# Kernel tuning notes

Hardware: AMD Instinct MI355X
Metric: run time of the kernel (lower is better)

The kernel has to match this reference:

```python
import jax, jax.numpy as jnp
import numpy as np
import math
from jax import lax

NUM_POS = 128        # random_choice in pos_neg_sampling
NUM_TOT = 256        # pos + (128 + negative_padding) always totals 256
POS_W = 10.0         # positive_weight in compute_loss


def _conv(x, w, b, pad):
    y = lax.conv_general_dilated(x, w, (1, 1), pad,
                                 dimension_numbers=('NCHW', 'OIHW', 'NCHW'))
    return y + b[None, :, None, None]


def make_anchor_box(img_h, img_w, gh, gw):
    # torch.range(0, W, W/(gw-1)) == inclusive linspace with gw points
    xs = jnp.linspace(0.0, float(img_w), gw)
    ys = jnp.linspace(0.0, float(img_h), gh)
    gx, gy = jnp.meshgrid(xs, ys, indexing='ij')          # (gw, gh) like torch.meshgrid
    xy = jnp.stack([gx.reshape(-1), gy.reshape(-1)], -1).reshape(gh, gw, 2)
    whs = []
    for area in (128 * 128, 256 * 256, 512 * 512):
        for wr, hr in ((1, 1), (2, 1), (1, 2)):
            u = math.sqrt(area / (wr * hr))
            whs.append((wr * u, hr * u))
    wh = jnp.asarray(whs, jnp.float32)                    # (9, 2)
    xy9 = jnp.broadcast_to(xy[:, :, None, :], (gh, gw, 9, 2))
    wh9 = jnp.broadcast_to(wh[None, None], (gh, gw, 9, 2))
    boxes = jnp.concatenate([xy9, xy9 + wh9], -1)         # x1,y1,x2,y2
    return boxes.reshape(-1, 4)


def pairwise_iou(t, a):
    # t: [T,4], a: [A,4], xyxy -> [T,A]
    lt = jnp.maximum(t[:, None, :2], a[None, :, :2])
    rb = jnp.minimum(t[:, None, 2:], a[None, :, 2:])
    wh = jnp.clip(rb - lt, 0.0)
    inter = wh[..., 0] * wh[..., 1]
    at = (t[:, 2] - t[:, 0]) * (t[:, 3] - t[:, 1])
    aa = (a[:, 2] - a[:, 0]) * (a[:, 3] - a[:, 1])
    return inter / (at[:, None] + aa[None, :] - inter)


def box_encode(anchor, bbox):
    awh = anchor[:, 2:] - anchor[:, :2]
    bwh = bbox[:, 2:] - bbox[:, :2]
    ac = anchor[:, :2] + awh / 2
    bc = bbox[:, :2] + bwh / 2
    dxy = (bc - ac) / awh
    dwh = jnp.log(bwh / awh)
    return jnp.concatenate([dxy, dwh], 1)


def rpn_forward(x, target, conv_w, conv_b, bbox_w, bbox_b, score_w, score_b,
                img_h, img_w):
    gh, gw = x.shape[-2], x.shape[-1]
    h = jax.nn.relu(_conv(x[None], conv_w, conv_b, 'SAME'))
    bbox = jax.nn.relu(_conv(h, bbox_w, bbox_b, 'VALID')).reshape(-1, 4)   # [A,4]
    score = jax.nn.relu(_conv(h, score_w, score_b, 'VALID')).reshape(-1, 2)  # [A,2]
    anchors = make_anchor_box(img_h, img_w, gh, gw)                        # [A,4]

    iou = pairwise_iou(target, anchors)                                    # [T,A]
    max_iou = iou.max(0)
    tgt_idx = jnp.argmax(iou, 0)

    # deterministic replacement for np.random.choice sampling (fixed shapes)
    pos_score = jnp.where(max_iou > 0.7, max_iou, -1.0)
    pos_vals, pos_idx = lax.top_k(pos_score, NUM_POS)
    pos_valid = pos_vals > 0.0
    n_pos = jnp.sum(pos_valid.astype(jnp.int32))

    neg_score = jnp.where(max_iou < 0.3, 1.0 - max_iou, -1.0)
    neg_vals, neg_idx = lax.top_k(neg_score, NUM_TOT)
    neg_valid = (neg_vals > 0.0) & (jnp.arange(NUM_TOT) < (NUM_TOT - n_pos))

    bbox_pred = bbox[pos_idx]                                              # [128,4]
    scores_sel = score[jnp.concatenate([pos_idx, neg_idx])]                # [384,2]
    valid = jnp.concatenate([pos_valid, neg_valid]).astype(jnp.float32)

    tgt_scores = jnp.concatenate([
        jnp.tile(jnp.asarray([[1.0, 0.0]], jnp.float32), (NUM_POS, 1)),
        jnp.tile(jnp.asarray([[0.0, 1.0]], jnp.float32), (NUM_TOT, 1))], 0)

    matched = target[tgt_idx[pos_idx]]
    treg = box_encode(anchors[pos_idx], matched)

    ce = -jnp.sum(tgt_scores * jax.nn.log_softmax(scores_sel, -1), -1)
    score_loss = jnp.sum(ce * valid) / jnp.maximum(jnp.sum(valid), 1.0)

    d = bbox_pred - treg
    sl1 = jnp.where(jnp.abs(d) < 1.0, 0.5 * d * d, jnp.abs(d) - 0.5)
    pm = pos_valid.astype(jnp.float32)[:, None]
    reg_loss = jnp.sum(sl1 * pm) / jnp.maximum(jnp.sum(pm) * 4.0, 1.0)

    return score_loss + POS_W * reg_loss


def setup_inputs():
    key = jax.random.key(0)
    ks = jax.random.split(key, 8)
    cin, gh, gw, nt = 512, 128, 128, 64
    x = jax.random.normal(ks[0], (cin, gh, gw), jnp.float32)
    cxy = jax.random.uniform(ks[1], (nt, 2), minval=300.0, maxval=1748.0)
    wh = jax.random.uniform(ks[2], (nt, 2), minval=64.0, maxval=512.0)
    target = jnp.concatenate([cxy - wh / 2, cxy + wh / 2], -1)
    conv_w = jax.random.normal(ks[3], (cin, cin, 3, 3), jnp.float32) * 0.02
    conv_b = jnp.zeros((cin,), jnp.float32)
    bbox_w = jax.random.normal(ks[4], (36, cin, 1, 1), jnp.float32) * 0.02
    bbox_b = jnp.zeros((36,), jnp.float32)
    score_w = jax.random.normal(ks[5], (18, cin, 1, 1), jnp.float32) * 0.02
    score_b = jnp.zeros((18,), jnp.float32)
    return {'x': x, 'target': target, 'conv_w': conv_w, 'conv_b': conv_b,
            'bbox_w': bbox_w, 'bbox_b': bbox_b, 'score_w': score_w,
            'score_b': score_b, 'img_h': 2048, 'img_w': 2048}


def reference(x, target, conv_w, conv_b, bbox_w, bbox_b, score_w, score_b,
              img_h, img_w):
    return rpn_forward(x, target, conv_w, conv_b, bbox_w, bbox_b,
                       score_w, score_b, img_h, img_w)
```

## Files before the change

kernel.cpp:

```cpp
#include <hip/hip_runtime.h>
#include <cstdint>
#include <cstddef>

typedef unsigned long long ull;
typedef __bf16 bf16x8 __attribute__((ext_vector_type(8)));
typedef float f32x4 __attribute__((ext_vector_type(4)));

#define NA     147456
#define NT     64
#define KDIM   4608
#define NTASK  1280
#define CAND_CAP 4096
#define KSPLIT 2
#define NSTEP  72
#define NIOUB  576
#define NTRB   2048
#define NPREP2 512
#define NZERO  197

#define OFF_WB2   0
#define OFF_XT    4718592
#define OFF_ZERO  22024192
#define OFF_H4    22302720
#define OFF_MIOU  32788480
#define OFF_CAND  33378304
#define OFF_CPB   34557952
#define OFF_CBZ   34560256
#define OFF_NPOS  34562560
#define OFF_TREG  34562576
#define OFF_TASKS 34564624

#define UANC 90.509667991878f
__device__ __constant__ float WKa[9] = {128.0f, 2.0f*UANC, UANC, 256.0f, 4.0f*UANC, 2.0f*UANC, 512.0f, 8.0f*UANC, 4.0f*UANC};
__device__ __constant__ float HKa[9] = {128.0f, UANC, 2.0f*UANC, 256.0f, 2.0f*UANC, 4.0f*UANC, 512.0f, 4.0f*UANC, 8.0f*UANC};

__device__ __forceinline__ float iou_one(float x1, float y1, float x2, float y2, float4 t) {
#pragma clang fp contract(off)
  float ltx = fmaxf(t.x, x1), lty = fmaxf(t.y, y1);
  float rbx = fminf(t.z, x2), rby = fminf(t.w, y2);
  float wx = fmaxf(rbx - ltx, 0.0f);
  float wy = fmaxf(rby - lty, 0.0f);
  float inter = wx * wy;
  float at = (t.z - t.x) * (t.w - t.y);
  float aa = (x2 - x1) * (y2 - y1);
  return inter / ((at + aa) - inter);
}

__device__ __forceinline__ unsigned short f2bf(float f) {
  unsigned int u = __float_as_uint(f);
  unsigned int r = (u + 0x7fffu + ((u >> 16) & 1u)) >> 16;
  return (unsigned short)r;
}

__device__ __forceinline__ int boff(int kcb) {
  int rk = kcb >> 6;
  int dy = (rk * 11) >> 5;
  int dxo = rk - dy * 3;
  return (dy * 130 + dxo) * 512 + (kcb & 63) * 8;
}

__global__ __launch_bounds__(256) void k_pi(const float* __restrict__ cw,
    unsigned short* __restrict__ Wb2, const float* __restrict__ x,
    unsigned short* __restrict__ xtb, unsigned short* __restrict__ zrg,
    const float* __restrict__ tgt, const int* __restrict__ imw,
    const int* __restrict__ imh, float* __restrict__ miou,
    ull* __restrict__ cand, int* __restrict__ cpb, int* __restrict__ cbz,
    float* __restrict__ out0) {
  __shared__ __align__(16) char smem[20480];
  int blk = blockIdx.x;
  int tid = threadIdx.x;
  if (blk >= NIOUB + NTRB + NPREP2) {
    int g = (blk - (NIOUB + NTRB + NPREP2)) * 256 + tid;
    uint4 z = {0u, 0u, 0u, 0u};
    if (g == 0) *out0 = 0.0f;
    if (g < 17408) {
      *(uint4*)(zrg + g * 8) = z;
    } else {
      int h = g - 17408;
      int pixi = h >> 6, j = h & 63;
      int yy, xx;
      if (pixi < 260) { yy = (pixi < 130) ? 0 : 129; xx = (pixi < 130) ? pixi : pixi - 130; }
      else { int p2 = pixi - 260; if (p2 < 128) { yy = 1 + p2; xx = 0; } else { yy = p2 - 127; xx = 129; } }
      *(uint4*)(xtb + (size_t)(yy * 130 + xx) * 512 + j * 8) = z;
    }
    return;
  }
  if (blk >= NIOUB + NTRB) {
    float* row = (float*)smem;
    int m = blk - (NIOUB + NTRB);
    const float* src = cw + (size_t)m * KDIM;
    for (int f = tid; f < KDIM; f += 256) {
      int cin = f / 9;
      row[cin * 10 + (f - cin * 9)] = src[f];
    }
    __syncthreads();
    for (int kc = tid; kc < 576; kc += 256) {
      int r = kc >> 6, c8 = kc & 63;
      int base = c8 * 80 + r;
      unsigned short o[8];
      #pragma unroll
      for (int j = 0; j < 8; ++j) o[j] = f2bf(row[base + j * 10]);
      *(uint4*)(Wb2 + ((size_t)kc * 512 + m) * 8) = *(const uint4*)o;
    }
    return;
  }
  if (blk >= NIOUB) {
    float* tile = (float*)smem;
    int tb = blk - NIOUB;
    int pix0 = (tb & 255) * 64;
    int cin0 = (tb >> 8) * 64;
    int pr = tid & 15, cr = tid >> 4;
    #pragma unroll
    for (int i = 0; i < 4; ++i) {
      int cin = cr + i * 16;
      float4 v = *(const float4*)(x + (size_t)(cin0 + cin) * 16384 + pix0 + pr * 4);
      tile[cin * 65 + pr * 4 + 0] = v.x;
      tile[cin * 65 + pr * 4 + 1] = v.y;
      tile[cin * 65 + pr * 4 + 2] = v.z;
      tile[cin * 65 + pr * 4 + 3] = v.w;
    }
    __syncthreads();
    #pragma unroll
    for (int i = 0; i < 4; ++i) {
      int pix = cr + i * 16;
      int plin = pix0 + pix;
      int py = plin >> 7, px = plin & 127;
      unsigned short o[4] = {f2bf(tile[(pr * 4 + 0) * 65 + pix]),
                             f2bf(tile[(pr * 4 + 1) * 65 + pix]),
                             f2bf(tile[(pr * 4 + 2) * 65 + pix]),
                             f2bf(tile[(pr * 4 + 3) * 65 + pix])};
      *(uint2*)(xtb + (size_t)((py + 1) * 130 + (px + 1)) * 512 + cin0 + pr * 4) = *(const uint2*)o;
    }
    return;
  }
  float4* ts = (float4*)smem;
  int* wz = (int*)(smem + 1024);
  int* wc = wz + 4;
  if (tid < NT) ts[tid] = ((const float4*)tgt)[tid];
  __syncthreads();
  int a = blk * 256 + tid;
  int k = a % 9;
  int pq = a / 9;
  int p = pq >> 7, q = pq & 127;
  float dx = (float)(*imw) / 127.0f;
  float dyl = (float)(*imh) / 127.0f;
  float x1 = (float)p * dx, y1 = (float)q * dyl;
  float x2 = x1 + WKa[k], y2 = y1 + HKa[k];
  float best = -1.0f;
  #pragma unroll 8
  for (int t = 0; t < NT; ++t) best = fmaxf(best, iou_one(x1, y1, x2, y2, ts[t]));
  miou[a] = best;
  int lane = tid & 63, w = tid >> 6;
  ull bz = __ballot(best == 0.0f);
  bool isc = best > 0.7f;
  ull bc = __ballot(isc);
  if (lane == 0) { wz[w] = (int)__popcll(bz); wc[w] = (int)__popcll(bc); }
  __syncthreads();
  if (tid == 0) {
    cbz[blk] = wz[0] + wz[1] + wz[2] + wz[3];
    cpb[blk] = wc[0] + wc[1] + wc[2] + wc[3];
  }
  if (isc) {
    int woff = 0;
    for (int i = 0; i < w; ++i) woff += wc[i];
    int rank = woff + (int)__popcll(bc & ((1ull << lane) - 1ull));
    cand[blk * 256 + rank] = ((ull)__float_as_uint(best) << 32) | (ull)(0xFFFFFFFFu - (unsigned)a);
  }
}

__global__ __launch_bounds__(256) void k_sel(const ull* __restrict__ cand,
    const int* __restrict__ cpb, const float* __restrict__ miou,
    const int* __restrict__ cbz, const float* __restrict__ tgt,
    const int* __restrict__ imw, const int* __restrict__ imh,
    int* __restrict__ nposp, float* __restrict__ treg, int* __restrict__ tasks) {
  __shared__ ull keys[CAND_CAP];
  __shared__ ull bnd[1024];
  __shared__ int hist[1024];
  __shared__ int cpbL[576];
  __shared__ int base576[577];
  __shared__ int wtot[4];
  __shared__ int selCnt, bndCnt, Tbin, mAbove;
  __shared__ int posi[128];
  __shared__ int npS;
  __shared__ int nzbase[145];
  __shared__ float4 ts[NT];
  __shared__ int negA[256];
  __shared__ int wsum[4];
  int tid = threadIdx.x;
  int lane = tid & 63;
  if (tid < NT) ts[tid] = ((const float4*)tgt)[tid];
  for (int i = tid; i < 576; i += 256) cpbL[i] = cpb[i];
  for (int i = tid; i < 1024; i += 256) hist[i] = 0;
  __syncthreads();
  int e0 = 0, e1 = 0, sA = 0, scanA = 0;
  if (tid < 192) {
    e0 = cpbL[3 * tid]; e1 = cpbL[3 * tid + 1]; int e2 = cpbL[3 * tid + 2];
    sA = e0 + e1 + e2;
    scanA = sA;
    for (int off = 1; off < 64; off <<= 1) {
      int v = __shfl_up(scanA, off);
      if (lane >= off) scanA += v;
    }
    if (lane == 63) wtot[tid >> 6] = scanA;
  }
  __syncthreads();
  if (tid < 192) {
    int w = tid >> 6;
    int woff = 0;
    for (int i = 0; i < w; ++i) woff += wtot[i];
    int excl = woff + scanA - sA;
    base576[3 * tid]     = excl;
    base576[3 * tid + 1] = excl + e0;
    base576[3 * tid + 2] = excl + e0 + e1;
    if (tid == 191) base576[576] = excl + sA;
  }
  __syncthreads();
  int cnt = base576[576]; if (cnt > CAND_CAP) cnt = CAND_CAP;
  for (int i = tid; i < CAND_CAP; i += 256) if (i >= cnt) keys[i] = 0ull;
  for (int rk = tid; rk < cnt; rk += 256) {
    int lo = 0, hi = 576;
    while (hi - lo > 1) { int mid = (lo + hi) >> 1; if (base576[mid] <= rk) lo = mid; else hi = mid; }
    keys[rk] = cand[lo * 256 + (rk - base576[lo])];
  }
  __syncthreads();
  if (cnt <= 128) {
    if (tid < cnt) posi[tid] = (int)(0xFFFFFFFFu - (unsigned)(keys[tid] & 0xFFFFFFFFull));
    if (tid == 0) { npS = cnt; *nposp = cnt; }
  } else {
    for (int i = tid; i < cnt; i += 256) {
      unsigned ib = (unsigned)(keys[i] >> 32);
      atomicAdd(&hist[(ib - 0x3F333334u) >> 13], 1);
    }
    __syncthreads();
    if (tid < 64) {
      int s = 0;
      #pragma unroll
      for (int t = 0; t < 16; ++t) s += hist[tid * 16 + t];
      int S = s;
      #pragma unroll
      for (int off = 1; off < 64; off <<= 1) {
        int u = __shfl_down(S, off);
        if (tid + off < 64) S += u;
      }
      ull mask = __ballot(S >= 128);
      int g = 63 - __clzll(mask);
      int aboveS = __shfl(S, (g + 1 < 64) ? g + 1 : 63);
      if (g == 63) aboveS = 0;
      if (tid == 0) {
        int run = aboveS, T = g * 16 + 15;
        for (int b = g * 16 + 15; b >= g * 16; --b) {
          int h = hist[b];
          if (run + h >= 128) { T = b; break; }
          run += h;
        }
        Tbin = T; mAbove = run; selCnt = 0; bndCnt = 0;
      }
    }
    __syncthreads();
    int T = Tbin, m = mAbove;
    for (int i = tid; i < cnt; i += 256) {
      ull kk = keys[i];
      unsigned ib = (unsigned)(kk >> 32);
      int b = (int)((ib - 0x3F333334u) >> 13);
      if (b > T) {
        int r = atomicAdd(&selCnt, 1);
        posi[r] = (int)(0xFFFFFFFFu - (unsigned)(kk & 0xFFFFFFFFull));
      } else if (b == T) {
        int r = atomicAdd(&bndCnt, 1);
        if (r < 1024) bnd[r] = kk;
      }
    }
    __syncthreads();
    int B = bndCnt;
    int need = 128 - m;
    if (B <= 1024) {
      int n2 = 2; while (n2 < B) n2 <<= 1;
      for (int i = tid; i < n2; i += 256) if (i >= B) bnd[i] = 0ull;
      for (int size = 2; size <= n2; size <<= 1)
        for (int stride = size >> 1; stride > 0; stride >>= 1) {
          __syncthreads();
          for (int t = tid; t < n2 / 2; t += 256) {
            int i = 2 * t - (t & (stride - 1));
            int j = i + stride;
            ull a = bnd[i], b2 = bnd[j];
            bool desc = ((i & size) == 0);
            if (desc ? (a < b2) : (a > b2)) { bnd[i] = b2; bnd[j] = a; }
          }
        }
      __syncthreads();
      if (tid < need) posi[m + tid] = (int)(0xFFFFFFFFu - (unsigned)(bnd[tid] & 0xFFFFFFFFull));
    } else {
      for (int size = 2; size <= CAND_CAP; size <<= 1)
        for (int stride = size >> 1; stride > 0; stride >>= 1) {
          __syncthreads();
          for (int t = tid; t < CAND_CAP / 2; t += 256) {
            int i = 2 * t - (t & (stride - 1));
            int j = i + stride;
            ull a = keys[i], b2 = keys[j];
            bool desc = ((i & size) == 0);
            if (desc ? (a < b2) : (a > b2)) { keys[i] = b2; keys[j] = a; }
          }
        }
      __syncthreads();
      if (tid < 128) posi[tid] = (int)(0xFFFFFFFFu - (unsigned)(keys[tid] & 0xFFFFFFFFull));
    }
    if (tid == 0) { npS = 128; *nposp = 128; }
  }
  __syncthreads();
  int np = npS;
  int sB = 0, scanB = 0;
  if (tid < 144) {
    int4 cz4 = *(const int4*)(cbz + 4 * tid);
    sB = cz4.x + cz4.y + cz4.z + cz4.w;
    scanB = sB;
    for (int off = 1; off < 64; off <<= 1) {
      int v = __shfl_up(scanB, off);
      if (lane >= off) scanB += v;
    }
    bool last = (tid < 128) ? (lane == 63) : (tid == 143);
    if (last) wsum[tid >> 6] = scanB;
  }
  __syncthreads();
  if (tid < 144) {
    int w = tid >> 6;
    int woff = 0;
    for (int i = 0; i < w; ++i) woff += wsum[i];
    nzbase[tid] = woff + scanB - sB;
    if (tid == 143) nzbase[144] = woff + scanB;
  }
  __syncthreads();
  int w = tid >> 6;
  for (int j = 0; j < 144; ++j) {
    if (nzbase[j] >= 256) break;
    int a0 = j * 1024 + tid * 4;
    float4 m4 = *(const float4*)(miou + a0);
    int f0 = (m4.x == 0.0f), f1 = (m4.y == 0.0f), f2 = (m4.z == 0.0f), f3 = (m4.w == 0.0f);
    int tsum = f0 + f1 + f2 + f3;
    int scan = tsum;
    for (int off = 1; off < 64; off <<= 1) {
      int v = __shfl_up(scan, off);
      if (lane >= off) scan += v;
    }
    if (lane == 63) wsum[w] = scan;
    __syncthreads();
    int woff = nzbase[j];
    for (int i = 0; i < w; ++i) woff += wsum[i];
    int r = woff + scan - tsum;
    if (f0) { if (r < 256) negA[r] = a0;     r++; }
    if (f1) { if (r < 256) negA[r] = a0 + 1; r++; }
    if (f2) { if (r < 256) negA[r] = a0 + 2; r++; }
    if (f3) { if (r < 256) negA[r] = a0 + 3;      }
    __syncthreads();
  }
  __syncthreads();
  if (tid < np) {
    int a = posi[tid];
    int k = a % 9; int pq = a / 9; int p = pq >> 7, q = pq & 127;
    float dx = (float)(*imw) / 127.0f, dyl = (float)(*imh) / 127.0f;
    float x1 = (float)p * dx, y1 = (float)q * dyl;
    float x2 = x1 + WKa[k], y2 = y1 + HKa[k];
    float best = -1.0f; int bt = 0;
    for (int t = 0; t < NT; ++t) {
      float v = iou_one(x1, y1, x2, y2, ts[t]);
      if (v > best) { best = v; bt = t; }
    }
    float4 m = ts[bt];
    float aw = x2 - x1, ah = y2 - y1;
    float acx = x1 + aw * 0.5f, acy = y1 + ah * 0.5f;
    float bwd = m.z - m.x, bhd = m.w - m.y;
    float bcx = m.x + bwd * 0.5f, bcy = m.y + bhd * 0.5f;
    treg[tid * 4 + 0] = (bcx - acx) / aw;
    treg[tid * 4 + 1] = (bcy - acy) / ah;
    treg[tid * 4 + 2] = logf(bwd / aw);
    treg[tid * 4 + 3] = logf(bhd / ah);
  }
  for (int t = tid; t < NTASK; t += 256) {
    int rec = 0;
    if (t < 768) {
      int s = t / 6, jj = t - s * 6;
      if (s < np) {
        int a = posi[s];
        int f, wr, xx;
        if (jj < 4) { f = 4 * a; wr = f >> 14; xx = (f & 127) + jj; }
        else        { f = 2 * a; wr = 36 + (f >> 14); xx = (f & 127) + (jj - 4); }
        int yy = (f >> 7) & 127;
        rec = (int)(0x80000000u | ((unsigned)wr << 16) | ((unsigned)yy << 8) | (unsigned)xx);
      }
    } else {
      int s = (t - 768) >> 1, jj = (t - 768) & 1;
      if (s < 256 - np) {
        int a = negA[s];
        int f = 2 * a; int wr = 36 + (f >> 14); int yy = (f >> 7) & 127; int xx = (f & 127) + jj;
        rec = (int)(0x80000000u | ((unsigned)wr << 16) | ((unsigned)yy << 8) | (unsigned)xx);
      }
    }
    tasks[t] = rec;
  }
}

__global__ __launch_bounds__(256) void k_mfma(const unsigned short* __restrict__ Wb2,
    const unsigned short* __restrict__ xtb, const unsigned short* __restrict__ zrg,
    const int* __restrict__ tasks, const int* __restrict__ nposp,
    float* __restrict__ H4) {
  int npos = *nposp;
  int tt0 = blockIdx.x * 128;
  int posend = 6 * npos, negend = 768 + 2 * (256 - npos);
  if (!((tt0 < posend) || ((tt0 + 128 > 768) && (tt0 < negend)))) return;
  int c0 = blockIdx.y * 128;
  int ks = blockIdx.z;
  int tid = threadIdx.x;
  int wave = tid >> 6, lane = tid & 63;
  int quad = lane >> 4, r = lane & 15;
  int m_base = c0 + (wave & 1) * 64;
  int n_base = tt0 + (wave >> 1) * 64;
  int kc0 = ks * 288 + quad;
  const bf16x8* Ab = (const bf16x8*)Wb2 + ((size_t)kc0 * 512 + m_base + r);

  const unsigned short* Bp[4];
  #pragma unroll
  for (int ni = 0; ni < 4; ++ni) {
    int rec = tasks[n_base + ni * 16 + r];
    int pix = (rec < 0) ? (((rec >> 8) & 127) * 130 + (rec & 127)) : 0;
    const unsigned short* base = (rec < 0) ? xtb : zrg;
    Bp[ni] = base + (size_t)pix * 512 + quad * 8;
  }
  int kcb = ks * 288;

  f32x4 acc[4][4];
  #pragma unroll
  for (int i = 0; i < 4; ++i)
    #pragma unroll
    for (int j = 0; j < 4; ++j) acc[i][j] = (f32x4){0.f, 0.f, 0.f, 0.f};

  bf16x8 a[4], b[4];
  #pragma unroll
  for (int mi = 0; mi < 4; ++mi) a[mi] = Ab[mi * 16];
  int ob0 = boff(kcb);
  #pragma unroll
  for (int ni = 0; ni < 4; ++ni) b[ni] = *(const bf16x8*)(Bp[ni] + ob0);

  for (int s = 0; s < NSTEP; ++s) {
    bf16x8 an[4], bn[4];
    if (s < NSTEP - 1) {
      const bf16x8* An = Ab + (size_t)(s + 1) * 4 * 512;
      int ob = boff(kcb + 4 * (s + 1));
      #pragma unroll
      for (int mi = 0; mi < 4; ++mi) an[mi] = An[mi * 16];
      #pragma unroll
      for (int ni = 0; ni < 4; ++ni) bn[ni] = *(const bf16x8*)(Bp[ni] + ob);
    }
    #pragma unroll
    for (int mi = 0; mi < 4; ++mi)
      #pragma unroll
      for (int ni = 0; ni < 4; ++ni)
        acc[mi][ni] = __builtin_amdgcn_mfma_f32_16x16x32_bf16(a[mi], b[ni], acc[mi][ni], 0, 0, 0);
    if (s < NSTEP - 1) {
      #pragma unroll
      for (int mi = 0; mi < 4; ++mi) a[mi] = an[mi];
      #pragma unroll
      for (int ni = 0; ni < 4; ++ni) b[ni] = bn[ni];
    }
  }
  size_t hb = (size_t)ks * NTASK;
  #pragma unroll
  for (int mi = 0; mi < 4; ++mi) {
    int c = m_base + mi * 16 + quad * 4;
    #pragma unroll
    for (int ni = 0; ni < 4; ++ni) {
      int t = n_base + ni * 16 + r;
      *(f32x4*)(H4 + (hb + t) * 512 + c) = acc[mi][ni];
    }
  }
}

__global__ __launch_bounds__(256) void k_out(const float* __restrict__ H4,
    const int* __restrict__ tasks,
    const float* __restrict__ cb, const float* __restrict__ bw,
    const float* __restrict__ bb, const float* __restrict__ sw,
    const float* __restrict__ sb, const float* __restrict__ treg,
    const int* __restrict__ nposp, float* __restrict__ out) {
  __shared__ float sOut[4];
  __shared__ float sContrib[4];
  int wave = threadIdx.x >> 6, lane = threadIdx.x & 63;
  int t = blockIdx.x * 4 + wave;
  int rec = tasks[t];
  float outval = 0.0f;
  if (rec < 0) {
    int wr = (rec >> 16) & 63;
    const float* wrow = (wr < 36) ? (bw + wr * 512) : (sw + (wr - 36) * 512);
    float s = 0.0f;
    #pragma unroll
    for (int it = 0; it < 8; ++it) {
      int c = it * 64 + lane;
      size_t o = (size_t)t * 512 + c;
      float hv = H4[o] + H4[o + 1280 * 512] + cb[c];
      s = fmaf(fmaxf(hv, 0.0f), wrow[c], s);
    }
    #pragma unroll
    for (int off = 32; off > 0; off >>= 1) s += __shfl_down(s, off);
    if (lane == 0) {
      float b = (wr < 36) ? bb[wr] : sb[wr - 36];
      outval = fmaxf(s + b, 0.0f);
    }
  }
  if (lane == 0) sOut[wave] = outval;
  __syncthreads();
  if (lane == 0) {
    float contrib = 0.0f;
    if (rec < 0) {
      if (t < 768) {
        int s6 = t / 6, j = t - s6 * 6;
        if (j < 4) {
          int np = *nposp;
          float d = outval - treg[s6 * 4 + j];
          float ad = fabsf(d);
          float sl1 = (ad < 1.0f) ? 0.5f * d * d : ad - 0.5f;
          contrib = 10.0f * sl1 / fmaxf(4.0f * (float)np, 1.0f);
        } else if (j == 4) {
          float s0 = outval, s1 = sOut[wave + 1];
          float mm = fmaxf(s0, s1);
          float lse = mm + logf(expf(s0 - mm) + expf(s1 - mm));
          contrib = (lse - s0) * (1.0f / 256.0f);
        }
      } else if (((t - 768) & 1) == 0) {
        float s0 = outval, s1 = sOut[wave + 1];
        float mm = fmaxf(s0, s1);
        float lse = mm + logf(expf(s0 - mm) + expf(s1 - mm));
        contrib = (lse - s1) * (1.0f / 256.0f);
      }
    }
    sContrib[wave] = contrib;
  }
  __syncthreads();
  if (threadIdx.x == 0) {
    float c = sContrib[0] + sContrib[1] + sContrib[2] + sContrib[3];
    if (c != 0.0f) atomicAdd(out, c);
  }
}

extern "C" void kernel_launch(void* const* d_in, const int* in_sizes, int n_in,
                              void* d_out, int out_size, void* d_ws, size_t ws_size,
                              hipStream_t stream) {
  const float* x   = (const float*)d_in[0];
  const float* tgt = (const float*)d_in[1];
  const float* cw  = (const float*)d_in[2];
  const float* cb  = (const float*)d_in[3];
  const float* bw  = (const float*)d_in[4];
  const float* bb  = (const float*)d_in[5];
  const float* sw  = (const float*)d_in[6];
  const float* sb  = (const float*)d_in[7];
  const int* imh   = (const int*)d_in[8];
  const int* imw   = (const int*)d_in[9];

  char* ws = (char*)d_ws;
  unsigned short* Wb2 = (unsigned short*)(ws + OFF_WB2);
  unsigned short* xtb = (unsigned short*)(ws + OFF_XT);
  unsigned short* zrg = (unsigned short*)(ws + OFF_ZERO);
  float* H4    = (float*)(ws + OFF_H4);
  float* miou  = (float*)(ws + OFF_MIOU);
  ull*   cand  = (ull*)(ws + OFF_CAND);
  int*   cpb   = (int*)(ws + OFF_CPB);
  int*   cbz   = (int*)(ws + OFF_CBZ);
  int*   nposp = (int*)(ws + OFF_NPOS);
  float* treg  = (float*)(ws + OFF_TREG);
  int*   tasks = (int*)(ws + OFF_TASKS);
  float* out   = (float*)d_out;

  k_pi   <<<dim3(NIOUB + NTRB + NPREP2 + NZERO), dim3(256), 0, stream>>>(cw, Wb2, x, xtb, zrg, tgt, imw, imh, miou, cand, cpb, cbz, out);
  k_sel  <<<dim3(1),              dim3(256), 0, stream>>>(cand, cpb, miou, cbz, tgt, imw, imh, nposp, treg, tasks);
  k_mfma <<<dim3(10, 4, KSPLIT),  dim3(256), 0, stream>>>(Wb2, xtb, zrg, tasks, nposp, H4);
  k_out  <<<dim3(320),            dim3(256), 0, stream>>>(H4, tasks, cb, bw, bb, sw, sb, treg, nposp, out);
}
```

Baseline: 175.6 us.

## Split conv GEMM K across four slices and deepen the register prefetch pipeline

Raises the K-split of the 3x3-conv MFMA GEMM from 2 to 4, doubling the block count so more CUs get work, while halving each block's K loop. The single-step register prefetch becomes a rotating 4-buffer scheme that loads three steps ahead, giving more latency hiding for the global loads. The output kernel now sums four partial-H slices instead of two, which adds partial-sum write and read traffic and raises register pressure in the GEMM kernel.

```diff
diff --git a/kernel.cpp b/kernel.cpp
--- a/kernel.cpp
+++ b/kernel.cpp
@@ -11,8 +11,8 @@
 #define KDIM   4608
 #define NTASK  1280
 #define CAND_CAP 4096
-#define KSPLIT 2
-#define NSTEP  72
+#define KSPLIT 4
+#define NSTEP  36
 #define NIOUB  576
 #define NTRB   2048
 #define NPREP2 512
@@ -413,7 +413,7 @@
   int quad = lane >> 4, r = lane & 15;
   int m_base = c0 + (wave & 1) * 64;
   int n_base = tt0 + (wave >> 1) * 64;
-  int kc0 = ks * 288 + quad;
+  int kc0 = ks * 144 + quad;
   const bf16x8* Ab = (const bf16x8*)Wb2 + ((size_t)kc0 * 512 + m_base + r);
 
   const unsigned short* Bp[4];
@@ -424,7 +424,7 @@
     const unsigned short* base = (rec < 0) ? xtb : zrg;
     Bp[ni] = base + (size_t)pix * 512 + quad * 8;
   }
-  int kcb = ks * 288;
+  int kcb = ks * 144;
 
   f32x4 acc[4][4];
   #pragma unroll
@@ -432,35 +432,38 @@
     #pragma unroll
     for (int j = 0; j < 4; ++j) acc[i][j] = (f32x4){0.f, 0.f, 0.f, 0.f};
 
-  bf16x8 a[4], b[4];
-  #pragma unroll
-  for (int mi = 0; mi < 4; ++mi) a[mi] = Ab[mi * 16];
-  int ob0 = boff(kcb);
-  #pragma unroll
-  for (int ni = 0; ni < 4; ++ni) b[ni] = *(const bf16x8*)(Bp[ni] + ob0);
-
-  for (int s = 0; s < NSTEP; ++s) {
-    bf16x8 an[4], bn[4];
-    if (s < NSTEP - 1) {
-      const bf16x8* An = Ab + (size_t)(s + 1) * 4 * 512;
-      int ob = boff(kcb + 4 * (s + 1));
-      #pragma unroll
-      for (int mi = 0; mi < 4; ++mi) an[mi] = An[mi * 16];
-      #pragma unroll
-      for (int ni = 0; ni < 4; ++ni) bn[ni] = *(const bf16x8*)(Bp[ni] + ob);
-    }
-    #pragma unroll
-    for (int mi = 0; mi < 4; ++mi)
-      #pragma unroll
-      for (int ni = 0; ni < 4; ++ni)
-        acc[mi][ni] = __builtin_amdgcn_mfma_f32_16x16x32_bf16(a[mi], b[ni], acc[mi][ni], 0, 0, 0);
-    if (s < NSTEP - 1) {
-      #pragma unroll
-      for (int mi = 0; mi < 4; ++mi) a[mi] = an[mi];
-      #pragma unroll
-      for (int ni = 0; ni < 4; ++ni) b[ni] = bn[ni];
-    }
-  }
+  bf16x8 a0[4], a1[4], a2[4], a3[4], b0[4], b1[4], b2[4], b3[4];
+
+#define LDSTEP(A, B, s)                                                        \
+  { const bf16x8* An = Ab + (size_t)(s) * 4 * 512;                             \
+    int ob = boff(kcb + 4 * (s));                                              \
+    _Pragma("unroll")                                                          \
+    for (int mi = 0; mi < 4; ++mi) A[mi] = An[mi * 16];                        \
+    _Pragma("unroll")                                                          \
+    for (int ni = 0; ni < 4; ++ni) B[ni] = *(const bf16x8*)(Bp[ni] + ob); }
+#define MMSTEP(A, B)                                                           \
+  { _Pragma("unroll")                                                          \
+    for (int mi = 0; mi < 4; ++mi)                                             \
+      _Pragma("unroll")                                                        \
+      for (int ni = 0; ni < 4; ++ni)                                           \
+        acc[mi][ni] = __builtin_amdgcn_mfma_f32_16x16x32_bf16(A[mi], B[ni], acc[mi][ni], 0, 0, 0); }
+
+  LDSTEP(a0, b0, 0)
+  LDSTEP(a1, b1, 1)
+  LDSTEP(a2, b2, 2)
+  for (int su = 0; su < NSTEP; su += 4) {
+    if (su + 3 < NSTEP) LDSTEP(a3, b3, su + 3)
+    MMSTEP(a0, b0)
+    if (su + 4 < NSTEP) LDSTEP(a0, b0, su + 4)
+    MMSTEP(a1, b1)
+    if (su + 5 < NSTEP) LDSTEP(a1, b1, su + 5)
+    MMSTEP(a2, b2)
+    if (su + 6 < NSTEP) LDSTEP(a2, b2, su + 6)
+    MMSTEP(a3, b3)
+  }
+#undef LDSTEP
+#undef MMSTEP
+
   size_t hb = (size_t)ks * NTASK;
   #pragma unroll
   for (int mi = 0; mi < 4; ++mi) {
@@ -493,7 +496,7 @@
     for (int it = 0; it < 8; ++it) {
       int c = it * 64 + lane;
       size_t o = (size_t)t * 512 + c;
-      float hv = H4[o] + H4[o + 1280 * 512] + cb[c];
+      float hv = H4[o] + H4[o + 1280 * 512] + H4[o + 2 * 1280 * 512] + H4[o + 3 * 1280 * 512] + cb[c];
       s = fmaf(fmaxf(hv, 0.0f), wrow[c], s);
     }
     #pragma unroll
```

Measured after the change: 155.7 us. 1.13x faster.
